# Kernel optimization log

Measured on AMD Instinct MI355X. Metric: run time of the kernel, lower is better.

## Reference

```python
import jax, jax.numpy as jnp
import numpy as np

E = 16        # n_routed_experts
K = 4         # num_experts_per_tok
G = 4         # n_group
TG = 2        # topk_group
NS = 2        # n_shared_experts
H = 1024      # hidden_size
I = 1408      # intermediate_size
SCALE = 1.0   # routed_scaling_factor


def _gate(x2d, gate_w, gate_bias):
    # x2d: [T,H], gate_w: [E,H], gate_bias: [E]
    T = x2d.shape[0]
    logits = x2d.astype(jnp.float32) @ gate_w.astype(jnp.float32).T   # [T,E]
    scores = jax.nn.sigmoid(logits)
    sfc = scores + gate_bias[None, :]
    # group scores = sum of top-2 expert scores within each group
    grp = sfc.reshape(T, G, E // G)
    top2, _ = jax.lax.top_k(grp, 2)
    group_scores = top2.sum(-1)                                       # [T,G]
    _, gidx = jax.lax.top_k(group_scores, TG)                         # [T,TG]
    gmask = jnp.zeros((T, G), sfc.dtype).at[jnp.arange(T)[:, None], gidx].set(1.0)
    smask = jnp.repeat(gmask, E // G, axis=1) > 0                     # [T,E]
    tmp = jnp.where(smask, sfc, 0.0)
    _, topk_idx = jax.lax.top_k(tmp, K)                               # [T,K]
    topk_w = jnp.take_along_axis(scores, topk_idx, axis=1)            # [T,K]
    topk_w = topk_w / (topk_w.sum(-1, keepdims=True) + 1e-20)         # norm_topk_prob
    return topk_idx, topk_w * SCALE


def setup_inputs() -> dict:
    key = jax.random.key(0)
    ks = jax.random.split(key, 8)
    bound = 1.0 / np.sqrt(H)  # kaiming_uniform(a=sqrt(5)) on [E,H]
    return {
        "hidden_states": jax.random.normal(ks[0], (1, 1024, H), jnp.float32),
        "gate_w": jax.random.uniform(ks[1], (E, H), jnp.float32, -bound, bound),
        "gate_bias": jnp.zeros((E,), jnp.float32),
        "gate_proj": jax.random.normal(ks[2], (E, I, H), jnp.float32) * 0.02,
        "up_proj": jax.random.normal(ks[3], (E, I, H), jnp.float32) * 0.02,
        "down_proj": jax.random.normal(ks[4], (E, H, I), jnp.float32) * 0.02,
        "shared_gate_w": jax.random.normal(ks[5], (I * NS, H), jnp.float32) * 0.02,
        "shared_up_w": jax.random.normal(ks[6], (I * NS, H), jnp.float32) * 0.02,
        "shared_down_w": jax.random.normal(ks[7], (H, I * NS), jnp.float32) * 0.02,
    }


def reference(hidden_states, gate_w, gate_bias, gate_proj, up_proj, down_proj,
              shared_gate_w, shared_up_w, shared_down_w):
    orig_shape = hidden_states.shape
    x = hidden_states.reshape(-1, H)                                  # [T,H]
    topk_idx, topk_w = _gate(x, gate_w, gate_bias)
    # per-token per-expert combine weight (top-k indices are unique per token,
    # so scatter-add combine == dense weighted sum)
    combine_w = (jax.nn.one_hot(topk_idx, E, dtype=x.dtype) * topk_w[..., None]).sum(1)  # [T,E]
    g = jnp.einsum('th,eih->tei', x, gate_proj)                       # [T,E,I]
    u = jnp.einsum('th,eih->tei', x, up_proj)
    act = jax.nn.silu(g) * u                                          # SwiGLU
    y = jnp.einsum('tei,ehi,te->th', act, down_proj, combine_w)       # [T,H]
    # shared experts
    sg = x @ shared_gate_w.T
    su = x @ shared_up_w.T
    y = y + (jax.nn.silu(sg) * su) @ shared_down_w.T
    return y.reshape(orig_shape)
```

## Files before the change

### kernel.cpp

```cpp
#include <hip/hip_runtime.h>
#include <hip/hip_bf16.h>

#define T_TOK 1024
#define H_DIM 1024
#define I_DIM 1408
#define NE 16
#define NEP 18
#define BM 256
#define LDB 40

typedef __attribute__((ext_vector_type(8))) __bf16 bf16x8;
typedef __attribute__((ext_vector_type(4))) float f32x4;

__device__ __forceinline__ bf16x8 cvt8(float4 a, float4 b) {
    bf16x8 r;
    r[0] = (__bf16)a.x; r[1] = (__bf16)a.y; r[2] = (__bf16)a.z; r[3] = (__bf16)a.w;
    r[4] = (__bf16)b.x; r[5] = (__bf16)b.y; r[6] = (__bf16)b.z; r[7] = (__bf16)b.w;
    return r;
}

__global__ __launch_bounds__(64) void gate_kernel(
    const float* __restrict__ x, const float* __restrict__ gw,
    const float* __restrict__ gb,
    int* __restrict__ counts, int* __restrict__ etok, float* __restrict__ ew)
{
    const int t = blockIdx.x;
    const int lane = threadIdx.x;
    float s[NE];
#pragma unroll
    for (int e = 0; e < NE; ++e) s[e] = 0.f;
    const float* xr = x + (size_t)t * H_DIM;
    for (int i = lane; i < H_DIM; i += 64) {
        float xv = xr[i];
#pragma unroll
        for (int e = 0; e < NE; ++e) s[e] += xv * gw[e * H_DIM + i];
    }
#pragma unroll
    for (int e = 0; e < NE; ++e) {
        for (int off = 32; off > 0; off >>= 1) s[e] += __shfl_xor(s[e], off);
    }
    if (lane == 0) {
        float scores[NE], sfc[NE];
#pragma unroll
        for (int e = 0; e < NE; ++e) {
            scores[e] = 1.f / (1.f + __expf(-s[e]));
            sfc[e] = scores[e] + gb[e];
        }
        float gsc[4];
#pragma unroll
        for (int g = 0; g < 4; ++g) {
            float m1 = -1e30f, m2 = -1e30f;
#pragma unroll
            for (int j = 0; j < 4; ++j) {
                float v = sfc[4 * g + j];
                if (v > m1) { m2 = m1; m1 = v; } else if (v > m2) { m2 = v; }
            }
            gsc[g] = m1 + m2;
        }
        int g1 = 0;
        for (int g = 1; g < 4; ++g) if (gsc[g] > gsc[g1]) g1 = g;
        int g2 = -1;
        for (int g = 0; g < 4; ++g) {
            if (g == g1) continue;
            if (g2 < 0 || gsc[g] > gsc[g2]) g2 = g;
        }
        float tmp[NE];
#pragma unroll
        for (int e = 0; e < NE; ++e) {
            int gg = e >> 2;
            tmp[e] = (gg == g1 || gg == g2) ? sfc[e] : 0.0f;
        }
        int idxs[4]; float wk[4]; float wsum = 0.f;
#pragma unroll
        for (int k = 0; k < 4; ++k) {
            int bi = 0;
            for (int e = 1; e < NE; ++e) if (tmp[e] > tmp[bi]) bi = e;
            idxs[k] = bi; wk[k] = scores[bi]; wsum += scores[bi];
            tmp[bi] = -1e30f;
        }
        float inv = 1.f / (wsum + 1e-20f);
        for (int k = 0; k < 4; ++k) {
            int e = idxs[k];
            int pos = atomicAdd(&counts[e], 1);
            etok[e * T_TOK + pos] = t;
            ew[e * T_TOK + pos] = wk[k] * inv;
        }
    }
}

__global__ __launch_bounds__(256) void cvtx_kernel(
    const float* __restrict__ x, __hip_bfloat16* __restrict__ x_bf)
{
    int i = (blockIdx.x * 256 + threadIdx.x) * 4;
    float4 v = ((const float4*)x)[i >> 2];
    x_bf[i + 0] = __float2bfloat16(v.x);
    x_bf[i + 1] = __float2bfloat16(v.y);
    x_bf[i + 2] = __float2bfloat16(v.z);
    x_bf[i + 3] = __float2bfloat16(v.w);
}

__global__ __launch_bounds__(256, 2) void gateup_kernel(
    const __hip_bfloat16* __restrict__ x_bf,
    const float* __restrict__ gproj, const float* __restrict__ uproj,
    const float* __restrict__ sgw, const float* __restrict__ suw,
    const int* __restrict__ counts, const int* __restrict__ etok,
    __hip_bfloat16* __restrict__ act, int e0)
{
    const int slot = blockIdx.y;
    const int e = e0 + slot;
    const int cnt = (e < NE) ? counts[e] : T_TOK;
    const int row0 = blockIdx.z * BM;
    if (row0 >= cnt) return;

    __shared__ int toks[BM];
    __shared__ __hip_bfloat16 Bg[2][64 * LDB];
    __shared__ __hip_bfloat16 Bu[2][64 * LDB];

    const int tid = threadIdx.x;
    {
        int r = row0 + tid;
        toks[tid] = (e < NE) ? ((r < cnt) ? etok[e * T_TOK + r] : 0) : r;
    }

    const int nb0 = blockIdx.x * 64;
    const float *wg, *wu;
    if (e < NE) {
        wg = gproj + (size_t)e * I_DIM * H_DIM;
        wu = uproj + (size_t)e * I_DIM * H_DIM;
    } else {
        wg = sgw + (size_t)(e - NE) * I_DIM * H_DIM;
        wu = suw + (size_t)(e - NE) * I_DIM * H_DIM;
    }
    const int scol = tid >> 2, sq = tid & 3;
    const float* sgp = wg + (size_t)(nb0 + scol) * H_DIM + sq * 8;
    const float* sup = wu + (size_t)(nb0 + scol) * H_DIM + sq * 8;
    const int lws = scol * LDB + sq * 8;

    const int lane = tid & 63;
    const int w = tid >> 6;
    const int col = lane & 15, kq = lane >> 4;

    __syncthreads();

    const __hip_bfloat16* ar[4];
#pragma unroll
    for (int mi = 0; mi < 4; ++mi)
        ar[mi] = x_bf + (size_t)toks[w * 64 + mi * 16 + col] * H_DIM + kq * 8;

    f32x4 accg[4][4], accu[4][4];
#pragma unroll
    for (int mi = 0; mi < 4; ++mi)
#pragma unroll
        for (int ni = 0; ni < 4; ++ni) {
            accg[mi][ni] = (f32x4){0.f, 0.f, 0.f, 0.f};
            accu[mi][ni] = (f32x4){0.f, 0.f, 0.f, 0.f};
        }

    float4 ga = ((const float4*)sgp)[0], gb4 = ((const float4*)sgp)[1];
    float4 ua = ((const float4*)sup)[0], ub = ((const float4*)sup)[1];

    for (int k = 0; k < 32; ++k) {
        const int buf = k & 1;
        *(bf16x8*)&Bg[buf][lws] = cvt8(ga, gb4);
        *(bf16x8*)&Bu[buf][lws] = cvt8(ua, ub);
        __syncthreads();
        if (k < 31) {
            const float* pg = sgp + (k + 1) * 32;
            const float* pu = sup + (k + 1) * 32;
            ga = ((const float4*)pg)[0]; gb4 = ((const float4*)pg)[1];
            ua = ((const float4*)pu)[0]; ub = ((const float4*)pu)[1];
        }
        bf16x8 a[4], bg[4], bu[4];
#pragma unroll
        for (int mi = 0; mi < 4; ++mi) a[mi] = *(const bf16x8*)(ar[mi] + k * 32);
#pragma unroll
        for (int ni = 0; ni < 4; ++ni) {
            bg[ni] = *(const bf16x8*)&Bg[buf][(ni * 16 + col) * LDB + kq * 8];
            bu[ni] = *(const bf16x8*)&Bu[buf][(ni * 16 + col) * LDB + kq * 8];
        }
#pragma unroll
        for (int mi = 0; mi < 4; ++mi)
#pragma unroll
            for (int ni = 0; ni < 4; ++ni) {
                accg[mi][ni] = __builtin_amdgcn_mfma_f32_16x16x32_bf16(a[mi], bg[ni], accg[mi][ni], 0, 0, 0);
                accu[mi][ni] = __builtin_amdgcn_mfma_f32_16x16x32_bf16(a[mi], bu[ni], accu[mi][ni], 0, 0, 0);
            }
        __syncthreads();
    }

#pragma unroll
    for (int mi = 0; mi < 4; ++mi)
#pragma unroll
        for (int ni = 0; ni < 4; ++ni)
#pragma unroll
            for (int r = 0; r < 4; ++r) {
                int lrow = w * 64 + mi * 16 + kq * 4 + r;
                int grow = row0 + lrow;
                float g = accg[mi][ni][r];
                float a = (grow < cnt) ? (g / (1.f + __expf(-g)) * accu[mi][ni][r]) : 0.f;
                act[((size_t)slot * T_TOK + grow) * I_DIM + nb0 + ni * 16 + col] =
                    __float2bfloat16(a);
            }
}

__global__ __launch_bounds__(256, 2) void down_kernel(
    const __hip_bfloat16* __restrict__ act,
    const float* __restrict__ dproj, const float* __restrict__ sdw,
    const int* __restrict__ counts, const int* __restrict__ etok,
    const float* __restrict__ ew, float* __restrict__ y, int e0)
{
    const int slot = blockIdx.y;
    const int e = e0 + slot;
    const int cnt = (e < NE) ? counts[e] : T_TOK;
    const int row0 = blockIdx.z * BM;
    if (row0 >= cnt) return;

    __shared__ int toks[BM];
    __shared__ float wts[BM];
    __shared__ __hip_bfloat16 Bd[2][64 * LDB];

    const int tid = threadIdx.x;
    {
        int r = row0 + tid;
        if (e < NE) {
            bool ok = r < cnt;
            toks[tid] = ok ? etok[e * T_TOK + r] : 0;
            wts[tid]  = ok ? ew[e * T_TOK + r] : 0.f;
        } else { toks[tid] = r; wts[tid] = 1.f; }
    }

    const int nb0 = blockIdx.x * 64;
    const float* wd;
    int wstride;
    if (e < NE) { wd = dproj + (size_t)e * H_DIM * I_DIM; wstride = I_DIM; }
    else        { wd = sdw + (size_t)(e - NE) * I_DIM;    wstride = 2 * I_DIM; }
    const int scol = tid >> 2, sq = tid & 3;
    const float* sdp = wd + (size_t)(nb0 + scol) * wstride + sq * 8;
    const int lws = scol * LDB + sq * 8;

    const int lane = tid & 63;
    const int w = tid >> 6;
    const int col = lane & 15, kq = lane >> 4;

    __syncthreads();

    const __hip_bfloat16* ar[4];
#pragma unroll
    for (int mi = 0; mi < 4; ++mi)
        ar[mi] = act + ((size_t)slot * T_TOK + row0 + w * 64 + mi * 16 + col) * I_DIM + kq * 8;

    f32x4 acc[4][4];
#pragma unroll
    for (int mi = 0; mi < 4; ++mi)
#pragma unroll
        for (int ni = 0; ni < 4; ++ni) acc[mi][ni] = (f32x4){0.f, 0.f, 0.f, 0.f};

    float4 da = ((const float4*)sdp)[0], db = ((const float4*)sdp)[1];

    for (int k = 0; k < I_DIM / 32; ++k) {
        const int buf = k & 1;
        *(bf16x8*)&Bd[buf][lws] = cvt8(da, db);
        __syncthreads();
        if (k < I_DIM / 32 - 1) {
            const float* pd = sdp + (k + 1) * 32;
            da = ((const float4*)pd)[0]; db = ((const float4*)pd)[1];
        }
        bf16x8 a[4], b[4];
#pragma unroll
        for (int mi = 0; mi < 4; ++mi) a[mi] = *(const bf16x8*)(ar[mi] + k * 32);
#pragma unroll
        for (int ni = 0; ni < 4; ++ni)
            b[ni] = *(const bf16x8*)&Bd[buf][(ni * 16 + col) * LDB + kq * 8];
#pragma unroll
        for (int mi = 0; mi < 4; ++mi)
#pragma unroll
            for (int ni = 0; ni < 4; ++ni)
                acc[mi][ni] = __builtin_amdgcn_mfma_f32_16x16x32_bf16(a[mi], b[ni], acc[mi][ni], 0, 0, 0);
        __syncthreads();
    }

#pragma unroll
    for (int mi = 0; mi < 4; ++mi)
#pragma unroll
        for (int ni = 0; ni < 4; ++ni)
#pragma unroll
            for (int r = 0; r < 4; ++r) {
                int lrow = w * 64 + mi * 16 + kq * 4 + r;
                int grow = row0 + lrow;
                if (grow < cnt)
                    atomicAdd(&y[(size_t)toks[lrow] * H_DIM + nb0 + ni * 16 + col],
                              acc[mi][ni][r] * wts[lrow]);
            }
}

extern "C" void kernel_launch(void* const* d_in, const int* in_sizes, int n_in,
                              void* d_out, int out_size, void* d_ws, size_t ws_size,
                              hipStream_t stream) {
    (void)in_sizes; (void)n_in; (void)out_size;
    const float* x  = (const float*)d_in[0];
    const float* gw = (const float*)d_in[1];
    const float* gb = (const float*)d_in[2];
    const float* gp = (const float*)d_in[3];
    const float* up = (const float*)d_in[4];
    const float* dp = (const float*)d_in[5];
    const float* sg = (const float*)d_in[6];
    const float* su = (const float*)d_in[7];
    const float* sd = (const float*)d_in[8];
    float* out = (float*)d_out;

    char* ws = (char*)d_ws;
    int*   counts = (int*)ws;
    int*   etok   = (int*)(ws + 256);
    float* ew     = (float*)(ws + 256 + 65536);
    __hip_bfloat16* x_bf = (__hip_bfloat16*)(ws + 131328);
    __hip_bfloat16* act  = (__hip_bfloat16*)(ws + 2228480);

    size_t fixed = 2228480;
    size_t per_e = (size_t)T_TOK * I_DIM * 2;
    int cap = NEP;
    if (ws_size < fixed + (size_t)NEP * per_e) {
        cap = (ws_size > fixed + per_e) ? (int)((ws_size - fixed) / per_e) : 1;
        if (cap < 1) cap = 1;
    }

    hipMemsetAsync(ws, 0, 256, stream);
    hipMemsetAsync(out, 0, (size_t)T_TOK * H_DIM * 4, stream);

    gate_kernel<<<dim3(T_TOK), dim3(64), 0, stream>>>(x, gw, gb, counts, etok, ew);
    cvtx_kernel<<<dim3(1024), dim3(256), 0, stream>>>(x, x_bf);

    for (int e0 = 0; e0 < NEP; e0 += cap) {
        int ne = NEP - e0 < cap ? NEP - e0 : cap;
        gateup_kernel<<<dim3(I_DIM / 64, ne, T_TOK / BM), dim3(256), 0, stream>>>(
            x_bf, gp, up, sg, su, counts, etok, act, e0);
        down_kernel<<<dim3(H_DIM / 64, ne, T_TOK / BM), dim3(256), 0, stream>>>(
            act, dp, sd, counts, etok, ew, out, e0);
    }
}
```

Before: 536.0 us.

## Load fp32 weights directly into MFMA B registers, dropping shared-memory staging

Both GEMM kernels stop staging converted bf16 weight tiles in LDS with double buffering and barriers. Each lane now reads its own fp32 weight fragment straight from global memory and converts it in registers right before the MFMA, with the k-loop unrolled by 2. This removes LDS traffic and per-iteration __syncthreads, but each weight element is now fetched and converted by all four waves instead of once per block. That raises global/L2 load volume and register use, and there is no software prefetch of the next tile. The down kernel's launch bound also goes to 3 blocks per SM.

```diff
diff --git a/kernel.cpp b/kernel.cpp
--- a/kernel.cpp
+++ b/kernel.cpp
@@ -7,7 +7,6 @@
 #define NE 16
 #define NEP 18
 #define BM 256
-#define LDB 40
 
 typedef __attribute__((ext_vector_type(8))) __bf16 bf16x8;
 typedef __attribute__((ext_vector_type(4))) float f32x4;
@@ -113,14 +112,12 @@
     if (row0 >= cnt) return;
 
     __shared__ int toks[BM];
-    __shared__ __hip_bfloat16 Bg[2][64 * LDB];
-    __shared__ __hip_bfloat16 Bu[2][64 * LDB];
-
     const int tid = threadIdx.x;
     {
         int r = row0 + tid;
         toks[tid] = (e < NE) ? ((r < cnt) ? etok[e * T_TOK + r] : 0) : r;
     }
+    __syncthreads();
 
     const int nb0 = blockIdx.x * 64;
     const float *wg, *wu;
@@ -131,21 +128,23 @@
         wg = sgw + (size_t)(e - NE) * I_DIM * H_DIM;
         wu = suw + (size_t)(e - NE) * I_DIM * H_DIM;
     }
-    const int scol = tid >> 2, sq = tid & 3;
-    const float* sgp = wg + (size_t)(nb0 + scol) * H_DIM + sq * 8;
-    const float* sup = wu + (size_t)(nb0 + scol) * H_DIM + sq * 8;
-    const int lws = scol * LDB + sq * 8;
 
     const int lane = tid & 63;
     const int w = tid >> 6;
     const int col = lane & 15, kq = lane >> 4;
 
-    __syncthreads();
-
     const __hip_bfloat16* ar[4];
 #pragma unroll
     for (int mi = 0; mi < 4; ++mi)
         ar[mi] = x_bf + (size_t)toks[w * 64 + mi * 16 + col] * H_DIM + kq * 8;
+
+    const float* brg[4];
+    const float* bru[4];
+#pragma unroll
+    for (int ni = 0; ni < 4; ++ni) {
+        brg[ni] = wg + (size_t)(nb0 + ni * 16 + col) * H_DIM + kq * 8;
+        bru[ni] = wu + (size_t)(nb0 + ni * 16 + col) * H_DIM + kq * 8;
+    }
 
     f32x4 accg[4][4], accu[4][4];
 #pragma unroll
@@ -156,27 +155,19 @@
             accu[mi][ni] = (f32x4){0.f, 0.f, 0.f, 0.f};
         }
 
-    float4 ga = ((const float4*)sgp)[0], gb4 = ((const float4*)sgp)[1];
-    float4 ua = ((const float4*)sup)[0], ub = ((const float4*)sup)[1];
-
+#pragma unroll 2
     for (int k = 0; k < 32; ++k) {
-        const int buf = k & 1;
-        *(bf16x8*)&Bg[buf][lws] = cvt8(ga, gb4);
-        *(bf16x8*)&Bu[buf][lws] = cvt8(ua, ub);
-        __syncthreads();
-        if (k < 31) {
-            const float* pg = sgp + (k + 1) * 32;
-            const float* pu = sup + (k + 1) * 32;
-            ga = ((const float4*)pg)[0]; gb4 = ((const float4*)pg)[1];
-            ua = ((const float4*)pu)[0]; ub = ((const float4*)pu)[1];
-        }
         bf16x8 a[4], bg[4], bu[4];
 #pragma unroll
         for (int mi = 0; mi < 4; ++mi) a[mi] = *(const bf16x8*)(ar[mi] + k * 32);
 #pragma unroll
         for (int ni = 0; ni < 4; ++ni) {
-            bg[ni] = *(const bf16x8*)&Bg[buf][(ni * 16 + col) * LDB + kq * 8];
-            bu[ni] = *(const bf16x8*)&Bu[buf][(ni * 16 + col) * LDB + kq * 8];
+            const float4* pg = (const float4*)(brg[ni] + k * 32);
+            const float4* pu = (const float4*)(bru[ni] + k * 32);
+            float4 g0 = pg[0], g1 = pg[1];
+            float4 u0 = pu[0], u1 = pu[1];
+            bg[ni] = cvt8(g0, g1);
+            bu[ni] = cvt8(u0, u1);
         }
 #pragma unroll
         for (int mi = 0; mi < 4; ++mi)
@@ -185,7 +176,6 @@
                 accg[mi][ni] = __builtin_amdgcn_mfma_f32_16x16x32_bf16(a[mi], bg[ni], accg[mi][ni], 0, 0, 0);
                 accu[mi][ni] = __builtin_amdgcn_mfma_f32_16x16x32_bf16(a[mi], bu[ni], accu[mi][ni], 0, 0, 0);
             }
-        __syncthreads();
     }
 
 #pragma unroll
@@ -203,7 +193,7 @@
             }
 }
 
-__global__ __launch_bounds__(256, 2) void down_kernel(
+__global__ __launch_bounds__(256, 3) void down_kernel(
     const __hip_bfloat16* __restrict__ act,
     const float* __restrict__ dproj, const float* __restrict__ sdw,
     const int* __restrict__ counts, const int* __restrict__ etok,
@@ -217,7 +207,6 @@
 
     __shared__ int toks[BM];
     __shared__ float wts[BM];
-    __shared__ __hip_bfloat16 Bd[2][64 * LDB];
 
     const int tid = threadIdx.x;
     {
@@ -228,55 +217,50 @@
             wts[tid]  = ok ? ew[e * T_TOK + r] : 0.f;
         } else { toks[tid] = r; wts[tid] = 1.f; }
     }
+    __syncthreads();
 
     const int nb0 = blockIdx.x * 64;
     const float* wd;
     int wstride;
     if (e < NE) { wd = dproj + (size_t)e * H_DIM * I_DIM; wstride = I_DIM; }
     else        { wd = sdw + (size_t)(e - NE) * I_DIM;    wstride = 2 * I_DIM; }
-    const int scol = tid >> 2, sq = tid & 3;
-    const float* sdp = wd + (size_t)(nb0 + scol) * wstride + sq * 8;
-    const int lws = scol * LDB + sq * 8;
 
     const int lane = tid & 63;
     const int w = tid >> 6;
     const int col = lane & 15, kq = lane >> 4;
 
-    __syncthreads();
-
     const __hip_bfloat16* ar[4];
 #pragma unroll
     for (int mi = 0; mi < 4; ++mi)
         ar[mi] = act + ((size_t)slot * T_TOK + row0 + w * 64 + mi * 16 + col) * I_DIM + kq * 8;
 
+    const float* brd[4];
+#pragma unroll
+    for (int ni = 0; ni < 4; ++ni)
+        brd[ni] = wd + (size_t)(nb0 + ni * 16 + col) * wstride + kq * 8;
+
     f32x4 acc[4][4];
 #pragma unroll
     for (int mi = 0; mi < 4; ++mi)
 #pragma unroll
         for (int ni = 0; ni < 4; ++ni) acc[mi][ni] = (f32x4){0.f, 0.f, 0.f, 0.f};
 
-    float4 da = ((const float4*)sdp)[0], db = ((const float4*)sdp)[1];
-
+#pragma unroll 2
     for (int k = 0; k < I_DIM / 32; ++k) {
-        const int buf = k & 1;
-        *(bf16x8*)&Bd[buf][lws] = cvt8(da, db);
-        __syncthreads();
-        if (k < I_DIM / 32 - 1) {
-            const float* pd = sdp + (k + 1) * 32;
-            da = ((const float4*)pd)[0]; db = ((const float4*)pd)[1];
-        }
         bf16x8 a[4], b[4];
 #pragma unroll
         for (int mi = 0; mi < 4; ++mi) a[mi] = *(const bf16x8*)(ar[mi] + k * 32);
 #pragma unroll
-        for (int ni = 0; ni < 4; ++ni)
-            b[ni] = *(const bf16x8*)&Bd[buf][(ni * 16 + col) * LDB + kq * 8];
+        for (int ni = 0; ni < 4; ++ni) {
+            const float4* pd = (const float4*)(brd[ni] + k * 32);
+            float4 d0 = pd[0], d1 = pd[1];
+            b[ni] = cvt8(d0, d1);
+        }
 #pragma unroll
         for (int mi = 0; mi < 4; ++mi)
 #pragma unroll
             for (int ni = 0; ni < 4; ++ni)
                 acc[mi][ni] = __builtin_amdgcn_mfma_f32_16x16x32_bf16(a[mi], b[ni], acc[mi][ni], 0, 0, 0);
-        __syncthreads();
     }
 
 #pragma unroll
```

Measured after the change: 858.2 us. +60.1%, slower.

## Use 4-stage LDS ring with single barrier per step and remap down grid

Applied to the files above, without the earlier changes.

Both GEMM kernels now keep four LDS buffers and prefetch weights two steps ahead in registers. This allows one barrier per k-step instead of two, using a raw s_barrier after an lgkmcnt wait. The down kernel switches to a flattened 1D grid that groups blocks so that 8 consecutive blocks share the same N-tile across different experts/row-tiles, which may help L2 locality and XCD distribution. Its occupancy hint is raised to 3 blocks per CU. The costs are more LDS and register pressure, and the correctness of the ring depends on the hand-placed barriers.

```diff
diff --git a/kernel.cpp b/kernel.cpp
--- a/kernel.cpp
+++ b/kernel.cpp
@@ -113,8 +113,8 @@
     if (row0 >= cnt) return;
 
     __shared__ int toks[BM];
-    __shared__ __hip_bfloat16 Bg[2][64 * LDB];
-    __shared__ __hip_bfloat16 Bu[2][64 * LDB];
+    __shared__ __align__(16) __hip_bfloat16 Bg[4][64 * LDB];
+    __shared__ __align__(16) __hip_bfloat16 Bu[4][64 * LDB];
 
     const int tid = threadIdx.x;
     {
@@ -156,27 +156,42 @@
             accu[mi][ni] = (f32x4){0.f, 0.f, 0.f, 0.f};
         }
 
-    float4 ga = ((const float4*)sgp)[0], gb4 = ((const float4*)sgp)[1];
-    float4 ua = ((const float4*)sup)[0], ub = ((const float4*)sup)[1];
-
-    for (int k = 0; k < 32; ++k) {
-        const int buf = k & 1;
-        *(bf16x8*)&Bg[buf][lws] = cvt8(ga, gb4);
-        *(bf16x8*)&Bu[buf][lws] = cvt8(ua, ub);
-        __syncthreads();
-        if (k < 31) {
-            const float* pg = sgp + (k + 1) * 32;
-            const float* pu = sup + (k + 1) * 32;
-            ga = ((const float4*)pg)[0]; gb4 = ((const float4*)pg)[1];
-            ua = ((const float4*)pu)[0]; ub = ((const float4*)pu)[1];
-        }
-        bf16x8 a[4], bg[4], bu[4];
+    float4 S0[4], S1[4];
+    S0[0] = ((const float4*)sgp)[0]; S0[1] = ((const float4*)sgp)[1];
+    S0[2] = ((const float4*)sup)[0]; S0[3] = ((const float4*)sup)[1];
+    {
+        const float* pg = sgp + 32; const float* pu = sup + 32;
+        S1[0] = ((const float4*)pg)[0]; S1[1] = ((const float4*)pg)[1];
+        S1[2] = ((const float4*)pu)[0]; S1[3] = ((const float4*)pu)[1];
+    }
+    *(bf16x8*)&Bg[0][lws] = cvt8(S0[0], S0[1]);
+    *(bf16x8*)&Bu[0][lws] = cvt8(S0[2], S0[3]);
+
+    auto gu_step = [&](int k, float4 (&wrS)[4], float4 (&ldS)[4],
+                       bool doStage, bool doWrite) {
+        bf16x8 a[4];
 #pragma unroll
         for (int mi = 0; mi < 4; ++mi) a[mi] = *(const bf16x8*)(ar[mi] + k * 32);
+        if (doStage) {
+            const float* pg = sgp + (k + 2) * 32;
+            const float* pu = sup + (k + 2) * 32;
+            ldS[0] = ((const float4*)pg)[0]; ldS[1] = ((const float4*)pg)[1];
+            ldS[2] = ((const float4*)pu)[0]; ldS[3] = ((const float4*)pu)[1];
+        }
+        if (doWrite) {
+            const int bw = (k + 1) & 3;
+            *(bf16x8*)&Bg[bw][lws] = cvt8(wrS[0], wrS[1]);
+            *(bf16x8*)&Bu[bw][lws] = cvt8(wrS[2], wrS[3]);
+        }
+        asm volatile("s_waitcnt lgkmcnt(0)" ::: "memory");
+        __builtin_amdgcn_s_barrier();
+        __builtin_amdgcn_sched_barrier(0);
+        const int br = k & 3;
+        bf16x8 bg[4], bu[4];
 #pragma unroll
         for (int ni = 0; ni < 4; ++ni) {
-            bg[ni] = *(const bf16x8*)&Bg[buf][(ni * 16 + col) * LDB + kq * 8];
-            bu[ni] = *(const bf16x8*)&Bu[buf][(ni * 16 + col) * LDB + kq * 8];
+            bg[ni] = *(const bf16x8*)&Bg[br][(ni * 16 + col) * LDB + kq * 8];
+            bu[ni] = *(const bf16x8*)&Bu[br][(ni * 16 + col) * LDB + kq * 8];
         }
 #pragma unroll
         for (int mi = 0; mi < 4; ++mi)
@@ -185,7 +200,11 @@
                 accg[mi][ni] = __builtin_amdgcn_mfma_f32_16x16x32_bf16(a[mi], bg[ni], accg[mi][ni], 0, 0, 0);
                 accu[mi][ni] = __builtin_amdgcn_mfma_f32_16x16x32_bf16(a[mi], bu[ni], accu[mi][ni], 0, 0, 0);
             }
-        __syncthreads();
+    };
+
+    for (int k = 0; k < 32; k += 2) {
+        gu_step(k,     S1, S0, k + 2 < 32, true);
+        gu_step(k + 1, S0, S1, k + 3 < 32, k + 2 < 32);
     }
 
 #pragma unroll
@@ -203,21 +222,28 @@
             }
 }
 
-__global__ __launch_bounds__(256, 2) void down_kernel(
+__global__ __launch_bounds__(256, 3) void down_kernel(
     const __hip_bfloat16* __restrict__ act,
     const float* __restrict__ dproj, const float* __restrict__ sdw,
     const int* __restrict__ counts, const int* __restrict__ etok,
-    const float* __restrict__ ew, float* __restrict__ y, int e0)
+    const float* __restrict__ ew, float* __restrict__ y, int e0, int ne)
 {
-    const int slot = blockIdx.y;
+    const int hw = blockIdx.x;
+    const int c = hw & 7, t = hw >> 3;
+    const int nbt = t & 15, gh = t >> 4;
+    const int g = c + 8 * gh;
+    if (g >= ne * 4) return;
+    const int slot = g % ne;
+    const int z = g / ne;
+
     const int e = e0 + slot;
     const int cnt = (e < NE) ? counts[e] : T_TOK;
-    const int row0 = blockIdx.z * BM;
+    const int row0 = z * BM;
     if (row0 >= cnt) return;
 
     __shared__ int toks[BM];
     __shared__ float wts[BM];
-    __shared__ __hip_bfloat16 Bd[2][64 * LDB];
+    __shared__ __align__(16) __hip_bfloat16 Bd[4][64 * LDB];
 
     const int tid = threadIdx.x;
     {
@@ -229,7 +255,7 @@
         } else { toks[tid] = r; wts[tid] = 1.f; }
     }
 
-    const int nb0 = blockIdx.x * 64;
+    const int nb0 = nbt * 64;
     const float* wd;
     int wstride;
     if (e < NE) { wd = dproj + (size_t)e * H_DIM * I_DIM; wstride = I_DIM; }
@@ -255,28 +281,46 @@
 #pragma unroll
         for (int ni = 0; ni < 4; ++ni) acc[mi][ni] = (f32x4){0.f, 0.f, 0.f, 0.f};
 
-    float4 da = ((const float4*)sdp)[0], db = ((const float4*)sdp)[1];
-
-    for (int k = 0; k < I_DIM / 32; ++k) {
-        const int buf = k & 1;
-        *(bf16x8*)&Bd[buf][lws] = cvt8(da, db);
-        __syncthreads();
-        if (k < I_DIM / 32 - 1) {
-            const float* pd = sdp + (k + 1) * 32;
-            da = ((const float4*)pd)[0]; db = ((const float4*)pd)[1];
-        }
-        bf16x8 a[4], b[4];
+    float4 S0[2], S1[2];
+    S0[0] = ((const float4*)sdp)[0]; S0[1] = ((const float4*)sdp)[1];
+    {
+        const float* pd = sdp + 32;
+        S1[0] = ((const float4*)pd)[0]; S1[1] = ((const float4*)pd)[1];
+    }
+    *(bf16x8*)&Bd[0][lws] = cvt8(S0[0], S0[1]);
+
+    auto d_step = [&](int k, float4 (&wrS)[2], float4 (&ldS)[2],
+                      bool doStage, bool doWrite) {
+        bf16x8 a[4];
 #pragma unroll
         for (int mi = 0; mi < 4; ++mi) a[mi] = *(const bf16x8*)(ar[mi] + k * 32);
+        if (doStage) {
+            const float* pd = sdp + (k + 2) * 32;
+            ldS[0] = ((const float4*)pd)[0]; ldS[1] = ((const float4*)pd)[1];
+        }
+        if (doWrite) {
+            const int bw = (k + 1) & 3;
+            *(bf16x8*)&Bd[bw][lws] = cvt8(wrS[0], wrS[1]);
+        }
+        asm volatile("s_waitcnt lgkmcnt(0)" ::: "memory");
+        __builtin_amdgcn_s_barrier();
+        __builtin_amdgcn_sched_barrier(0);
+        const int br = k & 3;
+        bf16x8 b[4];
 #pragma unroll
         for (int ni = 0; ni < 4; ++ni)
-            b[ni] = *(const bf16x8*)&Bd[buf][(ni * 16 + col) * LDB + kq * 8];
+            b[ni] = *(const bf16x8*)&Bd[br][(ni * 16 + col) * LDB + kq * 8];
 #pragma unroll
         for (int mi = 0; mi < 4; ++mi)
 #pragma unroll
             for (int ni = 0; ni < 4; ++ni)
                 acc[mi][ni] = __builtin_amdgcn_mfma_f32_16x16x32_bf16(a[mi], b[ni], acc[mi][ni], 0, 0, 0);
-        __syncthreads();
+    };
+
+    const int KS = I_DIM / 32;
+    for (int k = 0; k < KS; k += 2) {
+        d_step(k,     S1, S0, k + 2 < KS, true);
+        d_step(k + 1, S0, S1, k + 3 < KS, k + 2 < KS);
     }
 
 #pragma unroll
@@ -333,7 +377,8 @@
         int ne = NEP - e0 < cap ? NEP - e0 : cap;
         gateup_kernel<<<dim3(I_DIM / 64, ne, T_TOK / BM), dim3(256), 0, stream>>>(
             x_bf, gp, up, sg, su, counts, etok, act, e0);
-        down_kernel<<<dim3(H_DIM / 64, ne, T_TOK / BM), dim3(256), 0, stream>>>(
-            act, dp, sd, counts, etok, ew, out, e0);
-    }
-}
+        int Gp = ((ne * 4 + 7) / 8) * 8;
+        down_kernel<<<dim3(16 * Gp), dim3(256), 0, stream>>>(
+            act, dp, sd, counts, etok, ew, out, e0, ne);
+    }
+}
```

After: 488.0 us. 9.0% less time.
